# Kernel tuning notes

Hardware: AMD Instinct MI355X
Metric: run time of the kernel (lower is better)

The kernel has to match this reference:

```python
import jax, jax.numpy as jnp
import numpy as np

N, E, HS, HBS, L, SH, RBF, T, NZ, NH = 1024, 16384, 128, 32, 5, 25, 32, 50, 10, 4
HD = HS // NH
OUT = 14  # 3x0e + 2x1e + 1x2e -> 3 + 6 + 5
_rng = np.random.default_rng(7)
# fixed Clebsch-Gordan-style coupling tensor and expansion coefficients (deterministic constants)
CG = jnp.asarray((0.1 * _rng.normal(size=(SH, SH, SH))).astype(np.float32))
EXP = jnp.asarray((0.1 * _rng.normal(size=(SH, OUT, OUT))).astype(np.float32))
_SL = [(l * l, 2 * l + 1) for l in range(5)]  # per-l (offset, size) blocks in the 25-dim rep


def _real_sh(d):
    # real spherical harmonics l=0..4 of unit vectors d [E,3] -> [E,25]
    x, y, z = d[:, 0], d[:, 1], d[:, 2]
    x2, y2, z2 = x * x, y * y, z * z
    sh = [0.282095 * jnp.ones_like(x),
          0.488603 * y, 0.488603 * z, 0.488603 * x,
          1.092548 * x * y, 1.092548 * y * z, 0.315392 * (3 * z2 - 1), 1.092548 * x * z, 0.546274 * (x2 - y2),
          0.590044 * y * (3 * x2 - y2), 2.890611 * x * y * z, 0.457046 * y * (5 * z2 - 1),
          0.373176 * z * (5 * z2 - 3), 0.457046 * x * (5 * z2 - 1), 1.445306 * z * (x2 - y2),
          0.590044 * x * (x2 - 3 * y2),
          2.503343 * x * y * (x2 - y2), 1.770131 * y * z * (3 * x2 - y2), 0.946175 * x * y * (7 * z2 - 1),
          0.669047 * y * z * (7 * z2 - 3), 0.105786 * (35 * z2 * z2 - 30 * z2 + 3),
          0.669047 * x * z * (7 * z2 - 3), 0.473087 * (x2 - y2) * (7 * z2 - 1),
          1.770131 * x * z * (x2 - 3 * y2), 0.625836 * (x2 * x2 - 6 * x2 * y2 + y2 * y2)]
    return jnp.stack(sh, axis=-1)


def _rbf(r, cutoff=12.0, alpha=0.5):
    # exponential Bernstein radial basis with cosine cutoff, [E] -> [E,RBF]
    logf = np.concatenate([[0.0], np.cumsum(np.log(np.arange(1, RBF)))])
    logbinom = jnp.asarray((logf[RBF - 1] - logf - logf[::-1]).astype(np.float32))
    k = jnp.arange(RBF, dtype=jnp.float32)
    xr = jnp.exp(-alpha * r)[:, None]
    log1mx = jnp.log1p(-xr + 1e-7)
    b = jnp.exp(logbinom[None] + k[None] * (-alpha * r[:, None]) + (RBF - 1 - k)[None] * log1mx)
    fcut = 0.5 * (jnp.cos(jnp.pi * jnp.clip(r / cutoff, 0.0, 1.0)) + 1.0)
    return b * fcut[:, None]


def _mix(feat, W):
    # per-degree channel mixing: feat [*,C,25], W [5,C,D] -> [*,D,25]
    return jnp.concatenate([jnp.einsum('ncm,cd->ndm', feat[..., o:o + s], W[l])
                            for l, (o, s) in enumerate(_SL)], axis=-1)


def _forward(z, pos, edge_index, batch, t, step, embed, temb_T, temb_H, sig_W1, sig_b1, sig_W2, sig_b2,
             rad_W1, rad_b1, rad_W2, rad_b2, rad_W3, rad_b3, mix_W, Wq, Wk, Wii, Wij, path_ii, path_ij):
    n = z.shape[0]
    e = edge_index.shape[1]
    src, dst = edge_index[0], edge_index[1]
    vec = pos[src] - pos[dst]
    r = jnp.sqrt((vec * vec).sum(-1) + 1e-12)
    dvec = vec / r[:, None]
    rbf = _rbf(r)           # [E,32]
    sh = _real_sh(dvec)     # [E,25]
    nsc = embed[z]          # [N,HS]
    cat = jnp.concatenate([nsc, jnp.tile(temb_T[t][None], (n, 1)), jnp.tile(temb_H[step][None], (n, 1))], axis=-1)
    nsc = jax.nn.relu(cat @ sig_W1 + sig_b1) @ sig_W2 + sig_b2  # sigma_embedding
    x = jnp.zeros((n, HS, SH), jnp.float32).at[:, :, 0].set(nsc)  # scalar-initialized irrep features
    for l in range(L):
        # radial MLP -> per-edge per-channel tensor-product path weights
        h = jax.nn.silu(rbf @ rad_W1[l] + rad_b1[l])
        h = jax.nn.silu(h @ rad_W2[l] + rad_b2[l])
        w = h @ rad_W3[l] + rad_b3[l]                    # [E,HS]
        Tk = jnp.einsum('ej,ijk->eik', sh, CG)           # [E,25,25] CG-coupled SH operator
        msg = jnp.einsum('eci,eik->eck', x[src], Tk) * w[:, :, None]  # per-edge TP message [E,HS,25]
        agg = jax.ops.segment_sum(msg, dst, num_segments=n)
        y = _mix(agg, mix_W[l])
        # equivariant edge attention (scalars drive logits, full irreps are values)
        q = (x[:, :, 0] @ Wq[l]).reshape(n, NH, HD)
        kk = (x[:, :, 0] @ Wk[l]).reshape(n, NH, HD)
        logits = (q[dst] * kk[src]).sum(-1) * (1.0 / float(np.sqrt(HD)))  # [E,NH]
        m = jax.ops.segment_max(logits, dst, num_segments=n)
        m = jnp.where(jnp.isfinite(m), m, 0.0)
        a = jnp.exp(logits - m[dst])
        den = jax.ops.segment_sum(a, dst, num_segments=n)
        alpha = a / (den[dst] + 1e-9)
        v = x[src].reshape(e, NH, HD, SH)
        att = jax.ops.segment_sum(alpha[:, :, None, None] * v, dst, num_segments=n).reshape(n, HS, SH)
        x = x + y + att
        # gate nonlinearity: ssp/silu on scalars, sigmoid gate on higher-l blocks
        g = jax.nn.sigmoid(x[:, :, 0:1])
        x = jnp.concatenate([jax.nn.silu(x[:, :, 0:1]), x[:, :, 1:] * g], axis=-1)
    # expansion to hamiltonian blocks (3x0e+2x1e+1x2e -> 14x14)
    fii = _mix(x, Wii)                    # [N,HBS,25]
    fij = _mix(x[src] + x[dst], Wij)      # [E,HBS,25]
    w_ii = nsc @ path_ii                  # [N,HBS] path weights
    w_ij = jnp.concatenate([nsc[src], nsc[dst]], axis=-1) @ path_ij  # [E,HBS]
    H_ii = jnp.einsum('nd,ndm,mpq->npq', w_ii, fii, EXP)  # [N,14,14]
    H_ij = jnp.einsum('ed,edm,mpq->epq', w_ij, fij, EXP)  # [E,14,14]
    return H_ii, H_ij


def setup_inputs() -> dict:
    key = jax.random.key(0)
    ks = jax.random.split(key, 40)
    def nrm(i, shape, s):
        return (jax.random.normal(ks[i], shape) * s).astype(jnp.float32)
    inp = {}
    inp['z'] = jax.random.randint(ks[0], (N,), 0, NZ)
    inp['pos'] = nrm(1, (N, 3), 3.0)
    inp['edge_index'] = jax.random.randint(ks[2], (2, E), 0, N)
    inp['batch'] = jnp.sort(jax.random.randint(ks[3], (N,), 0, 8))
    inp['t'] = 25
    inp['step'] = 10
    inp['embed'] = nrm(4, (NZ, HS), 1.0)
    inp['temb_T'] = nrm(5, (T, HS), 1.0)
    inp['temb_H'] = nrm(6, (T, HS), 1.0)
    inp['sig_W1'] = nrm(7, (3 * HS, HS), (3 * HS) ** -0.5)
    inp['sig_b1'] = jnp.zeros((HS,), jnp.float32)
    inp['sig_W2'] = nrm(8, (HS, HS), HS ** -0.5)
    inp['sig_b2'] = jnp.zeros((HS,), jnp.float32)
    inp['rad_W1'] = nrm(9, (L, RBF, 64), RBF ** -0.5)
    inp['rad_b1'] = jnp.zeros((L, 64), jnp.float32)
    inp['rad_W2'] = nrm(10, (L, 64, 64), 64 ** -0.5)
    inp['rad_b2'] = jnp.zeros((L, 64), jnp.float32)
    inp['rad_W3'] = nrm(11, (L, 64, HS), 64 ** -0.5)
    inp['rad_b3'] = jnp.zeros((L, HS), jnp.float32)
    inp['mix_W'] = nrm(12, (L, 5, HS, HS), HS ** -0.5)
    inp['Wq'] = nrm(13, (L, HS, HS), HS ** -0.5)
    inp['Wk'] = nrm(14, (L, HS, HS), HS ** -0.5)
    inp['Wii'] = nrm(15, (5, HS, HBS), HS ** -0.5)
    inp['Wij'] = nrm(16, (5, HS, HBS), HS ** -0.5)
    inp['path_ii'] = nrm(17, (HS, HBS), HS ** -0.5)
    inp['path_ij'] = nrm(18, (2 * HS, HBS), (2 * HS) ** -0.5)
    return inp


def reference(z, pos, edge_index, batch, t, step, embed, temb_T, temb_H, sig_W1, sig_b1, sig_W2, sig_b2,
              rad_W1, rad_b1, rad_W2, rad_b2, rad_W3, rad_b3, mix_W, Wq, Wk, Wii, Wij, path_ii, path_ij):
    return _forward(z, pos, edge_index, batch, t, step, embed, temb_T, temb_H, sig_W1, sig_b1, sig_W2, sig_b2,
                    rad_W1, rad_b1, rad_W2, rad_b2, rad_W3, rad_b3, mix_W, Wq, Wk, Wii, Wij, path_ii, path_ij)
```

## Files before the change

kernel.cpp:

```cpp
#include <hip/hip_runtime.h>
#include <cstdint>
#include <cmath>
#include <cstddef>

constexpr int NN   = 1024;
constexpr int NE   = 16384;
constexpr int HSZ  = 128;
constexpr int NSH  = 25;
constexpr int NRBF = 32;
constexpr int NLAY = 5;
constexpr int XSZ  = HSZ * NSH;
constexpr int HII_SZ = NN * 196;
constexpr int TKP  = 800;


constexpr size_t OFF_CONSTS = 0;
constexpr size_t OFF_X    = 20560;
constexpr size_t OFF_AGG  = OFF_X    + (size_t)NN * XSZ;
constexpr size_t OFF_ATT  = OFF_AGG  + (size_t)NN * XSZ;
constexpr size_t OFF_X0   = OFF_ATT  + (size_t)NN * XSZ;
constexpr size_t OFF_NSC  = OFF_X0   + (size_t)NN * HSZ;
constexpr size_t OFF_Q    = OFF_NSC  + (size_t)NN * HSZ;
constexpr size_t OFF_K    = OFF_Q    + (size_t)NN * HSZ;
constexpr size_t OFF_RBF  = OFF_K    + (size_t)NN * HSZ;
constexpr size_t OFF_SH   = OFF_RBF  + (size_t)NE * NRBF;
constexpr size_t OFF_TK   = OFF_SH   + (size_t)NE * NSH;
constexpr size_t OFF_WRAD = OFF_TK   + (size_t)NE * TKP;
constexpr size_t OFF_INT  = OFF_WRAD + (size_t)NE * HSZ;
constexpr size_t NEED_BYTES = OFF_INT * 4 + (size_t)(1024 + 1025 + 1024 + 16384) * 4;

namespace qhc {

struct Pcg64 {
  unsigned __int128 state, inc;
  static unsigned __int128 mult() {
    return (((unsigned __int128)2549297995355413924ULL) << 64) | 4865540595714422341ULL;
  }
  void step() { state = state * mult() + inc; }
  uint64_t next64() {
    step();
    uint64_t hi = (uint64_t)(state >> 64), lo = (uint64_t)state;
    uint64_t x = hi ^ lo;
    unsigned rot = (unsigned)(state >> 122);
    return (x >> rot) | (x << ((64u - rot) & 63u));
  }
  double nextd() { return (double)(next64() >> 11) * (1.0 / 9007199254740992.0); }
};

struct HostConsts {
  float buf[20560];
  HostConsts() {
    const uint32_t INIT_A = 0x43b0d7e5u, MULT_A = 0x931e8875u;
    const uint32_t INIT_B = 0x8b51f9ddu, MULT_B = 0x58f38dedu;
    uint32_t pool[4];
    uint32_t hc = INIT_A;
    auto hashf = [&](uint32_t v) -> uint32_t {
      v ^= hc; hc *= MULT_A; v *= hc; v ^= v >> 16; return v;
    };
    auto mixf = [](uint32_t x, uint32_t y) -> uint32_t {
      uint32_t r = x * 0xca01f9ddu - y * 0x4973f715u;
      r ^= r >> 16;
      return r;
    };
    pool[0] = hashf(7u);
    for (int i = 1; i < 4; i++) pool[i] = hashf(0u);
    for (int s = 0; s < 4; s++)
      for (int d = 0; d < 4; d++)
        if (s != d) pool[d] = mixf(pool[d], hashf(pool[s]));
    uint32_t st32[8];
    uint32_t hb = INIT_B;
    for (int i = 0; i < 8; i++) {
      uint32_t v = pool[i % 4];
      v ^= hb; hb *= MULT_B; v *= hb; v ^= v >> 16;
      st32[i] = v;
    }
    uint64_t w0 = st32[0] | ((uint64_t)st32[1] << 32);
    uint64_t w1 = st32[2] | ((uint64_t)st32[3] << 32);
    uint64_t w2 = st32[4] | ((uint64_t)st32[5] << 32);
    uint64_t w3 = st32[6] | ((uint64_t)st32[7] << 32);
    unsigned __int128 seed = (((unsigned __int128)w0) << 64) | w1;
    unsigned __int128 incs = (((unsigned __int128)w2) << 64) | w3;
    Pcg64 g;
    g.state = 0; g.inc = (incs << 1) | 1;
    g.step(); g.state += seed; g.step();
    double wi[256], fi[256]; uint64_t ki[256];
    {
      const double m1 = 4503599627370496.0;
      double dn = 3.6541528853610087963519472518, tn = dn, vn = 0.00492867323399941;
      double q = vn / std::exp(-0.5 * dn * dn);
      ki[0] = (uint64_t)((dn / q) * m1); ki[1] = 0;
      wi[0] = q / m1; wi[255] = dn / m1;
      fi[0] = 1.0; fi[255] = std::exp(-0.5 * dn * dn);
      for (int i = 254; i >= 1; i--) {
        dn = std::sqrt(-2.0 * std::log(vn / dn + std::exp(-0.5 * dn * dn)));
        ki[i + 1] = (uint64_t)((dn / tn) * m1);
        tn = dn;
        fi[i] = std::exp(-0.5 * dn * dn);
        wi[i] = dn / m1;
      }
    }
    const double ZR = 3.6541528853610087963519472518;
    const double ZIR = 0.27366123732975827203338247596;
    auto stdnorm = [&]() -> double {
      for (;;) {
        uint64_t r = g.next64();
        int idx = (int)(r & 0xff);
        r >>= 8;
        int sign = (int)(r & 1);
        uint64_t rabs = (r >> 1) & 0x000fffffffffffffULL;
        double xv = (double)rabs * wi[idx];
        if (sign) xv = -xv;
        if (rabs < ki[idx]) return xv;
        if (idx == 0) {
          for (;;) {
            double xx = -ZIR * std::log1p(-g.nextd());
            double yy = -std::log1p(-g.nextd());
            if (yy + yy > xx * xx)
              return ((rabs >> 8) & 1) ? -(ZR + xx) : (ZR + xx);
          }
        } else {
          if (((fi[idx - 1] - fi[idx]) * g.nextd() + fi[idx]) < std::exp(-0.5 * xv * xv))
            return xv;
        }
      }
    };
    for (int i = 0; i < 15625 + 4900; i++) buf[i] = (float)(0.1 * stdnorm());
    double logf[32]; logf[0] = 0.0;
    for (int i = 1; i < 32; i++) logf[i] = logf[i - 1] + std::log((double)i);
    for (int k = 0; k < 32; k++) buf[15625 + 4900 + k] = (float)(logf[31] - logf[k] - logf[31 - k]);
    buf[20557] = buf[20558] = buf[20559] = 0.f;
  }
};
static HostConsts g_hc;
}

__device__ __forceinline__ float siluf(float a) { return a / (1.f + expf(-a)); }

__global__ __launch_bounds__(256) void qh_geom(
    const float* __restrict__ pos, const int* __restrict__ ei,
    const float* __restrict__ lbn, float* __restrict__ rbf, float* __restrict__ sh) {
  int e = blockIdx.x * 256 + threadIdx.x;
  if (e >= NE) return;
  int s = ei[e], d = ei[NE + e];
  float vx = pos[s * 3 + 0] - pos[d * 3 + 0];
  float vy = pos[s * 3 + 1] - pos[d * 3 + 1];
  float vz = pos[s * 3 + 2] - pos[d * 3 + 2];
  float r = sqrtf(vx * vx + vy * vy + vz * vz + 1e-12f);
  float inv = 1.0f / r;
  float x = vx * inv, y = vy * inv, z = vz * inv;
  float x2 = x * x, y2 = y * y, z2 = z * z;
  float* sp = sh + (size_t)e * NSH;
  sp[0] = 0.282095f;
  sp[1] = 0.488603f * y;
  sp[2] = 0.488603f * z;
  sp[3] = 0.488603f * x;
  sp[4] = 1.092548f * x * y;
  sp[5] = 1.092548f * y * z;
  sp[6] = 0.315392f * (3.f * z2 - 1.f);
  sp[7] = 1.092548f * x * z;
  sp[8] = 0.546274f * (x2 - y2);
  sp[9] = 0.590044f * y * (3.f * x2 - y2);
  sp[10] = 2.890611f * x * y * z;
  sp[11] = 0.457046f * y * (5.f * z2 - 1.f);
  sp[12] = 0.373176f * z * (5.f * z2 - 3.f);
  sp[13] = 0.457046f * x * (5.f * z2 - 1.f);
  sp[14] = 1.445306f * z * (x2 - y2);
  sp[15] = 0.590044f * x * (x2 - 3.f * y2);
  sp[16] = 2.503343f * x * y * (x2 - y2);
  sp[17] = 1.770131f * y * z * (3.f * x2 - y2);
  sp[18] = 0.946175f * x * y * (7.f * z2 - 1.f);
  sp[19] = 0.669047f * y * z * (7.f * z2 - 3.f);
  sp[20] = 0.105786f * (35.f * z2 * z2 - 30.f * z2 + 3.f);
  sp[21] = 0.669047f * x * z * (7.f * z2 - 3.f);
  sp[22] = 0.473087f * (x2 - y2) * (7.f * z2 - 1.f);
  sp[23] = 1.770131f * x * z * (x2 - 3.f * y2);
  sp[24] = 0.625836f * (x2 * x2 - 6.f * x2 * y2 + y2 * y2);
  float xr = expf(-0.5f * r);
  float l1 = log1pf(-xr + 1e-7f);
  float fc = 0.5f * (cosf(3.14159265358979323846f * fminf(r * (1.0f / 12.0f), 1.0f)) + 1.0f);
  float* rp = rbf + (size_t)e * NRBF;
  for (int k = 0; k < NRBF; k++) {
    float b = expf(lbn[k] + (float)k * (-0.5f * r) + (float)(NRBF - 1 - k) * l1);
    rp[k] = b * fc;
  }
}

__global__ __launch_bounds__(256) void qh_tk(
    const float* __restrict__ sh, const float* __restrict__ CG, float* __restrict__ Tkp) {
  __shared__ float shl[32 * NSH];
  int e0 = blockIdx.x * 32;
  int t = threadIdx.x;
  for (int i = t; i < 32 * NSH; i += 256) shl[i] = sh[(size_t)e0 * NSH + i];
  for (int i = t; i < 32 * TKP; i += 256) Tkp[(size_t)e0 * TKP + i] = 0.f;
  __syncthreads();
  for (int ik = t; ik < NSH * NSH; ik += 256) {
    int i = ik / NSH, k = ik % NSH;
    int pos = i * 32 + k + (k >= 7) + 2 * (k >= 13) + 2 * (k >= 19);
    float cg[NSH];
#pragma unroll
    for (int j = 0; j < NSH; j++) cg[j] = CG[i * 625 + j * NSH + k];
    for (int ee = 0; ee < 32; ee++) {
      float acc = 0.f;
#pragma unroll
      for (int j = 0; j < NSH; j++) acc += shl[ee * NSH + j] * cg[j];
      Tkp[(size_t)(e0 + ee) * TKP + pos] = acc;
    }
  }
}

__global__ __launch_bounds__(128) void qh_nsc(
    const int* __restrict__ z, const int* __restrict__ tptr, const int* __restrict__ sptr,
    const float* __restrict__ embed, const float* __restrict__ tT, const float* __restrict__ tH,
    const float* __restrict__ W1, const float* __restrict__ b1,
    const float* __restrict__ W2, const float* __restrict__ b2,
    float* __restrict__ nsc, float* __restrict__ x, float* __restrict__ x0) {
  __shared__ float cat[384];
  __shared__ float h[128];
  int nd = blockIdx.x, d = threadIdx.x;
  int zz = z[nd], tt = tptr[0], st = sptr[0];
  cat[d] = embed[zz * HSZ + d];
  cat[128 + d] = tT[tt * HSZ + d];
  cat[256 + d] = tH[st * HSZ + d];
  __syncthreads();
  float a = b1[d];
  for (int c = 0; c < 384; c++) a += cat[c] * W1[c * HSZ + d];
  h[d] = fmaxf(a, 0.f);
  __syncthreads();
  a = b2[d];
  for (int c = 0; c < 128; c++) a += h[c] * W2[c * HSZ + d];
  nsc[nd * HSZ + d] = a;
  x0[nd * HSZ + d] = a;
  float* xr = x + (size_t)nd * XSZ + d;
  xr[0] = a;
  for (int m = 1; m < NSH; m++) xr[m * 128] = 0.f;
}

__global__ __launch_bounds__(256) void qh_zero(int* counts) {
  int i = blockIdx.x * 256 + threadIdx.x;
  if (i < NN) counts[i] = 0;
}
__global__ __launch_bounds__(256) void qh_count(const int* __restrict__ ei, int* counts) {
  int e = blockIdx.x * 256 + threadIdx.x;
  if (e < NE) atomicAdd(&counts[ei[NE + e]], 1);
}
__global__ __launch_bounds__(1024) void qh_scan(const int* __restrict__ counts,
                                                int* starts, int* cursor) {
  __shared__ int tmp[NN];
  int t = threadIdx.x;
  tmp[t] = counts[t];
  __syncthreads();
  for (int ofs = 1; ofs < NN; ofs <<= 1) {
    int v = (t >= ofs) ? tmp[t - ofs] : 0;
    __syncthreads();
    tmp[t] += v;
    __syncthreads();
  }
  starts[t + 1] = tmp[t];
  if (t == 0) starts[0] = 0;
  cursor[t] = (t == 0) ? 0 : tmp[t - 1];
}
__global__ __launch_bounds__(256) void qh_scatter(const int* __restrict__ ei,
                                                  int* cursor, int* perm) {
  int e = blockIdx.x * 256 + threadIdx.x;
  if (e < NE) {
    int d = ei[NE + e];
    int pos = atomicAdd(&cursor[d], 1);
    perm[pos] = e;
  }
}

__global__ __launch_bounds__(256) void qh_rad(
    const float* __restrict__ rbf,
    const float* __restrict__ W1, const float* __restrict__ b1,
    const float* __restrict__ W2, const float* __restrict__ b2,
    const float* __restrict__ W3, const float* __restrict__ b3,
    float* __restrict__ wrad) {
  __shared__ float w1l[2048], w2l[4096], w3l[8192];
  __shared__ float rl[4][32], h1[4][64], h2[4][64];
  int t = threadIdx.x;
  for (int i = t; i < 2048; i += 256) w1l[i] = W1[i];
  for (int i = t; i < 4096; i += 256) w2l[i] = W2[i];
  for (int i = t; i < 8192; i += 256) w3l[i] = W3[i];
  __syncthreads();
  int e0 = blockIdx.x * 16;
  for (int q = 0; q < 4; q++) {
    int eb = e0 + q * 4;
    if (t < 128) rl[t >> 5][t & 31] = rbf[(size_t)(eb + (t >> 5)) * NRBF + (t & 31)];
    __syncthreads();
    {
      int eg = t >> 6, u = t & 63;
      float a = b1[u];
      for (int c = 0; c < 32; c++) a += rl[eg][c] * w1l[c * 64 + u];
      h1[eg][u] = siluf(a);
    }
    __syncthreads();
    {
      int eg = t >> 6, u = t & 63;
      float a = b2[u];
      for (int c = 0; c < 64; c++) a += h1[eg][c] * w2l[c * 64 + u];
      h2[eg][u] = siluf(a);
    }
    __syncthreads();
#pragma unroll
    for (int p = 0; p < 2; p++) {
      int eg = (t >> 7) + p * 2, u = t & 127;
      float a = b3[u];
      for (int c = 0; c < 64; c++) a += h2[eg][c] * w3l[c * 128 + u];
      wrad[(size_t)(eb + eg) * HSZ + u] = a;
    }
    __syncthreads();
  }
}

__global__ __launch_bounds__(256) void qh_qk(
    const float* __restrict__ x0, const float* __restrict__ Wq, const float* __restrict__ Wk,
    float* __restrict__ q, float* __restrict__ kk) {
  __shared__ float xl[128];
  int nd = blockIdx.x, t = threadIdx.x;
  if (t < 128) xl[t] = x0[nd * HSZ + t];
  __syncthreads();
  int d = t & 127;
  const float* W = (t < 128) ? Wq : Wk;
  float a = 0.f;
  for (int c = 0; c < 128; c++) a += xl[c] * W[c * HSZ + d];
  if (t < 128) q[nd * HSZ + d] = a;
  else kk[nd * HSZ + d] = a;
}

__global__ __launch_bounds__(256) void qh_logit(
    const float* __restrict__ q, const float* __restrict__ kk,
    const int* __restrict__ ei, float* __restrict__ logits) {
  int t = threadIdx.x;
  int e = blockIdx.x * 2 + (t >> 7);
  int c = t & 127;
  int s = ei[e], d = ei[NE + e];
  float p = q[d * HSZ + c] * kk[s * HSZ + c];
#pragma unroll
  for (int m = 16; m >= 1; m >>= 1) p += __shfl_xor(p, m);
  if ((c & 31) == 0) logits[e * 4 + (c >> 5)] = p * 0.17677669529663687f;
}

__global__ __launch_bounds__(64) void qh_soft(
    const float* __restrict__ logits, const int* __restrict__ starts,
    const int* __restrict__ perm, float* __restrict__ alpha) {
  int nd = blockIdx.x, t = threadIdx.x;
  int hh = t >> 4, l = t & 15;
  int jb = starts[nd], je = starts[nd + 1];
  float m = -1e30f;
  for (int j = jb + l; j < je; j += 16) m = fmaxf(m, logits[perm[j] * 4 + hh]);
#pragma unroll
  for (int s = 1; s < 16; s <<= 1) m = fmaxf(m, __shfl_xor(m, s));
  float den = 0.f;
  for (int j = jb + l; j < je; j += 16) den += expf(logits[perm[j] * 4 + hh] - m);
#pragma unroll
  for (int s = 1; s < 16; s <<= 1) den += __shfl_xor(den, s);
  float inv = 1.f / (den + 1e-9f);
  for (int j = jb + l; j < je; j += 16) {
    int e = perm[j];
    alpha[e * 4 + hh] = expf(logits[e * 4 + hh] - m) * inv;
  }
}

__global__ __launch_bounds__(256, 8) void qh_msgatt(
    const float* __restrict__ x, const float* __restrict__ Tkp,
    const float* __restrict__ wrad, const float* __restrict__ alpha,
    const int* __restrict__ starts, const int* __restrict__ perm,
    const int* __restrict__ ei,
    float* __restrict__ agg, float* __restrict__ att) {
  __shared__ float xs[2][1600];
  __shared__ float wl[2][64];
  int nd = blockIdx.x >> 1, h = blockIdx.x & 1;
  int t = threadIdx.x;
  int cl = t & 63, q4 = t >> 6;
  int q4u = __builtin_amdgcn_readfirstlane(q4);
  int c = h * 64 + cl;
  int k0 = (q4 == 0) ? 0 : (1 + 6 * q4);
  int nk = (q4 == 0) ? 7 : 6;
  float am[7], aa[7];
#pragma unroll
  for (int u = 0; u < 7; u++) { am[u] = 0.f; aa[u] = 0.f; }
  int jb = starts[nd], je = starts[nd + 1];

  float rx[7], rw = 0.f;
  if (jb < je) {
    int e = perm[jb], s = ei[e];
#pragma unroll
    for (int u = 0; u < 6; u++) {
      int i = t + u * 256;
      rx[u] = x[(size_t)s * XSZ + (i >> 6) * 128 + h * 64 + (i & 63)];
    }
    if (t < 64) rx[6] = x[(size_t)s * XSZ + 24 * 128 + h * 64 + t];
    if (t < 64) rw = wrad[(size_t)e * HSZ + h * 64 + t];
#pragma unroll
    for (int u = 0; u < 6; u++) xs[0][t + u * 256] = rx[u];
    if (t < 64) xs[0][1536 + t] = rx[6];
    if (t < 64) wl[0][t] = rw;
  }
  __syncthreads();
  for (int j = jb; j < je; j++) {
    int cur = (j - jb) & 1, nxt = cur ^ 1;
    int e = perm[j];
    int eu = __builtin_amdgcn_readfirstlane(e);
    const float* tkr = Tkp + (size_t)eu * TKP + q4u * 8;
    float al = alpha[e * 4 + (c >> 5)];
    bool more = (j + 1 < je);
    if (more) {
      int e2 = perm[j + 1], s2 = ei[e2];
#pragma unroll
      for (int u = 0; u < 6; u++) {
        int i = t + u * 256;
        rx[u] = x[(size_t)s2 * XSZ + (i >> 6) * 128 + h * 64 + (i & 63)];
      }
      if (t < 64) rx[6] = x[(size_t)s2 * XSZ + 24 * 128 + h * 64 + t];
      if (t < 64) rw = wrad[(size_t)e2 * HSZ + h * 64 + t];
    }
    float wc = wl[cur][cl];
#pragma unroll 5
    for (int i = 0; i < NSH; i++) {
      float xw = xs[cur][i * 64 + cl] * wc;
      float4 t0 = *(const float4*)(tkr + i * 32);
      float4 t1 = *(const float4*)(tkr + i * 32 + 4);
      am[0] += xw * t0.x; am[1] += xw * t0.y; am[2] += xw * t0.z; am[3] += xw * t0.w;
      am[4] += xw * t1.x; am[5] += xw * t1.y; am[6] += xw * t1.z;
    }
#pragma unroll
    for (int u = 0; u < 7; u++)
      if (u < nk) aa[u] += al * xs[cur][(k0 + u) * 64 + cl];
    __syncthreads();
    if (more) {
#pragma unroll
      for (int u = 0; u < 6; u++) xs[nxt][t + u * 256] = rx[u];
      if (t < 64) xs[nxt][1536 + t] = rx[6];
      if (t < 64) wl[nxt][t] = rw;
    }
    __syncthreads();
  }
#pragma unroll
  for (int u = 0; u < 7; u++)
    if (u < nk) {
      agg[(size_t)nd * XSZ + (k0 + u) * 128 + c] = am[u];
      att[(size_t)nd * XSZ + (k0 + u) * 128 + c] = aa[u];
    }
}

__global__ __launch_bounds__(256) void qh_mixgemm(
    const float* __restrict__ mixW, float* __restrict__ agg) {
  __shared__ float Wl[8192];
  __shared__ float Al[4096];
  int b = blockIdx.x, t = threadIdx.x;
  int lb, cum;
  if (b < 32)       { lb = 0; cum = 0; }
  else if (b < 128) { lb = 1; cum = 32; }
  else if (b < 288) { lb = 2; cum = 128; }
  else if (b < 512) { lb = 3; cum = 288; }
  else              { lb = 4; cum = 512; }
  int sl = 2 * lb + 1, o = lb * lb;
  int row0 = (b - cum) * 32;
  const float* W = mixW + lb * 16384;
  for (int i = t; i < 4096; i += 256) {
    int r = i >> 7, cc = i & 127;
    int gr = row0 + r, n = gr / sl, m = o + gr - n * sl;
    Al[i] = agg[(size_t)n * XSZ + m * 128 + cc];
  }
  int dl = t & 63, rg = t >> 6;
  float out[2][8];
  for (int p = 0; p < 2; p++) {
    __syncthreads();
    for (int i = t; i < 8192; i += 256) {
      int cc = i >> 6, d2 = i & 63;
      Wl[i] = W[cc * 128 + p * 64 + d2];
    }
    __syncthreads();
    float acc[8];
#pragma unroll
    for (int r = 0; r < 8; r++) acc[r] = 0.f;
    for (int cc = 0; cc < 128; cc++) {
      float w = Wl[cc * 64 + dl];
#pragma unroll
      for (int r = 0; r < 8; r++) acc[r] += Al[(rg * 8 + r) * 128 + cc] * w;
    }
#pragma unroll
    for (int r = 0; r < 8; r++) out[p][r] = acc[r];
  }
#pragma unroll
  for (int p = 0; p < 2; p++)
#pragma unroll
    for (int r = 0; r < 8; r++) {
      int gr = row0 + rg * 8 + r, n = gr / sl, m = o + gr - n * sl;
      agg[(size_t)n * XSZ + m * 128 + p * 64 + dl] = out[p][r];
    }
}

__global__ __launch_bounds__(256) void qh_gate(
    const float* __restrict__ y, const float* __restrict__ att,
    float* __restrict__ x, float* __restrict__ x0) {
  __shared__ float v0l[128];
  int nd = blockIdx.x, t = threadIdx.x;
  int d = t & 127, mh = t >> 7;
  int m0 = mh ? 13 : 0, nm = mh ? 12 : 13;
  float v[13];
  size_t base = (size_t)nd * XSZ + (size_t)m0 * 128 + d;
#pragma unroll
  for (int u = 0; u < 13; u++)
    if (u < nm) v[u] = x[base + (size_t)u * 128] + y[base + (size_t)u * 128] + att[base + (size_t)u * 128];
  if (mh == 0) v0l[d] = v[0];
  __syncthreads();
  float g = 1.f / (1.f + expf(-v0l[d]));
#pragma unroll
  for (int u = 0; u < 13; u++)
    if (u < nm) x[base + (size_t)u * 128] = v[u] * g;
  if (mh == 0) x0[nd * HSZ + d] = v[0] * g;
}

__global__ __launch_bounds__(256) void qh_prep(
    const float* __restrict__ x, const float* __restrict__ nsc,
    const float* __restrict__ Wii, const float* __restrict__ Wij,
    const float* __restrict__ pii, const float* __restrict__ pij,
    const float* __restrict__ EXPc,
    float* __restrict__ fm, float* __restrict__ awb, float* __restrict__ out) {
  __shared__ float xl[XSZ];
  __shared__ float nl[128];
  __shared__ float wc[4096];
  __shared__ float fml[800];
  __shared__ float wiil[32];
  __shared__ float gl[25];
  int nd = blockIdx.x, t = threadIdx.x;
  for (int i = t; i < XSZ; i += 256) xl[i] = x[(size_t)nd * XSZ + i];
  if (t < 128) nl[t] = nsc[nd * HSZ + t];
  __syncthreads();
  if (t < 32) {
    float a = 0.f;
    for (int cc = 0; cc < 128; cc++) a += nl[cc] * pii[cc * 32 + t];
    wiil[t] = a;
  } else if (t < 96) {
    int d = (t - 32) & 31;
    int half = (t - 32) >> 5;
    const float* pp = pij + (half ? 128 * 32 : 0);
    float a = 0.f;
    for (int cc = 0; cc < 128; cc++) a += nl[cc] * pp[cc * 32 + d];
    awb[nd * 64 + half * 32 + d] = a;
  }
  for (int lb = 0; lb < 5; lb++) {
    __syncthreads();
    for (int i = t; i < 4096; i += 256) wc[i] = Wii[lb * 4096 + i];
    __syncthreads();
    int o = lb * lb, sl = 2 * lb + 1;
    for (int idx = t; idx < 32 * sl; idx += 256) {
      int d = idx & 31, m = o + (idx >> 5);
      float a = 0.f;
      for (int cc = 0; cc < 128; cc++) a += xl[m * 128 + cc] * wc[cc * 32 + d];
      fml[d * NSH + m] = a;
    }
  }
  __syncthreads();
  if (t < 25) {
    float a = 0.f;
#pragma unroll
    for (int d = 0; d < 32; d++) a += wiil[d] * fml[d * NSH + t];
    gl[t] = a;
  }
  __syncthreads();
  if (t < 196) {
    float a = 0.f;
#pragma unroll
    for (int m = 0; m < 25; m++) a += gl[m] * EXPc[m * 196 + t];
    out[(size_t)nd * 196 + t] = a;
  }
  for (int lb = 0; lb < 5; lb++) {
    __syncthreads();
    for (int i = t; i < 4096; i += 256) wc[i] = Wij[lb * 4096 + i];
    __syncthreads();
    int o = lb * lb, sl = 2 * lb + 1;
    for (int idx = t; idx < 32 * sl; idx += 256) {
      int d = idx & 31, m = o + (idx >> 5);
      float a = 0.f;
      for (int cc = 0; cc < 128; cc++) a += xl[m * 128 + cc] * wc[cc * 32 + d];
      fm[(size_t)nd * 800 + d * NSH + m] = a;
    }
  }
}

__global__ __launch_bounds__(256) void qh_fij2(
    const int* __restrict__ ei, const float* __restrict__ fm,
    const float* __restrict__ awb, const float* __restrict__ EXPc,
    float* __restrict__ out) {
  __shared__ float fsum[800], wsum[32], gl[25];
  int e = blockIdx.x, t = threadIdx.x;
  int s = ei[e], d2 = ei[NE + e];
  for (int i = t; i < 800; i += 256)
    fsum[i] = fm[(size_t)s * 800 + i] + fm[(size_t)d2 * 800 + i];
  if (t < 32) wsum[t] = awb[s * 64 + t] + awb[d2 * 64 + 32 + t];
  __syncthreads();
  if (t < 25) {
    float a = 0.f;
#pragma unroll
    for (int d = 0; d < 32; d++) a += wsum[d] * fsum[d * NSH + t];
    gl[t] = a;
  }
  __syncthreads();
  if (t < 196) {
    float a = 0.f;
#pragma unroll
    for (int m = 0; m < 25; m++) a += gl[m] * EXPc[m * 196 + t];
    out[HII_SZ + (size_t)e * 196 + t] = a;
  }
}

extern "C" void kernel_launch(void* const* d_in, const int* in_sizes, int n_in,
                              void* d_out, int out_size, void* d_ws, size_t ws_size,
                              hipStream_t stream) {
  (void)in_sizes; (void)n_in; (void)out_size;
  if (ws_size < NEED_BYTES) return;

  const int*   z    = (const int*)d_in[0];
  const float* pos  = (const float*)d_in[1];
  const int*   ei   = (const int*)d_in[2];
  const int*   tptr = (const int*)d_in[4];
  const int*   sptr = (const int*)d_in[5];
  const float* embed= (const float*)d_in[6];
  const float* tT   = (const float*)d_in[7];
  const float* tH   = (const float*)d_in[8];
  const float* sW1  = (const float*)d_in[9];
  const float* sb1  = (const float*)d_in[10];
  const float* sW2  = (const float*)d_in[11];
  const float* sb2  = (const float*)d_in[12];
  const float* rW1  = (const float*)d_in[13];
  const float* rb1  = (const float*)d_in[14];
  const float* rW2  = (const float*)d_in[15];
  const float* rb2  = (const float*)d_in[16];
  const float* rW3  = (const float*)d_in[17];
  const float* rb3  = (const float*)d_in[18];
  const float* mixW = (const float*)d_in[19];
  const float* Wq   = (const float*)d_in[20];
  const float* Wk   = (const float*)d_in[21];
  const float* Wii  = (const float*)d_in[22];
  const float* Wij  = (const float*)d_in[23];
  const float* pii  = (const float*)d_in[24];
  const float* pij  = (const float*)d_in[25];

  float* ws = (float*)d_ws;
  float* CGd   = ws + OFF_CONSTS;
  float* EXPd  = CGd + 15625;
  float* LBNd  = CGd + 15625 + 4900;
  float* x     = ws + OFF_X;
  float* agg   = ws + OFF_AGG;
  float* att   = ws + OFF_ATT;
  float* x0    = ws + OFF_X0;
  float* nsc   = ws + OFF_NSC;
  float* qarr  = ws + OFF_Q;
  float* karr  = ws + OFF_K;
  float* rbf   = ws + OFF_RBF;
  float* sh    = ws + OFF_SH;
  float* Tkp   = ws + OFF_TK;
  float* wrad  = ws + OFF_WRAD;
  float* logits = ws + OFF_SH;
  float* alphaA = ws + OFF_SH + 65536;
  float* fm     = ws + OFF_AGG;
  float* awb    = ws + OFF_AGG + 819200;
  int* ibase   = (int*)(ws + OFF_INT);
  int* counts  = ibase;
  int* starts  = ibase + 1024;
  int* cursor  = ibase + 1024 + 1025;
  int* perm    = ibase + 1024 + 1025 + 1024;
  float* outp  = (float*)d_out;

  hipMemcpyAsync(CGd, qhc::g_hc.buf, 20557 * sizeof(float), hipMemcpyHostToDevice, stream);

  qh_geom<<<NE / 256, 256, 0, stream>>>(pos, ei, LBNd, rbf, sh);
  qh_tk<<<NE / 32, 256, 0, stream>>>(sh, CGd, Tkp);
  qh_nsc<<<NN, 128, 0, stream>>>(z, tptr, sptr, embed, tT, tH, sW1, sb1, sW2, sb2, nsc, x, x0);
  qh_zero<<<NN / 256, 256, 0, stream>>>(counts);
  qh_count<<<NE / 256, 256, 0, stream>>>(ei, counts);
  qh_scan<<<1, 1024, 0, stream>>>(counts, starts, cursor);
  qh_scatter<<<NE / 256, 256, 0, stream>>>(ei, cursor, perm);

  for (int l = 0; l < NLAY; l++) {
    qh_rad<<<NE / 16, 256, 0, stream>>>(rbf,
        rW1 + (size_t)l * 32 * 64, rb1 + (size_t)l * 64,
        rW2 + (size_t)l * 64 * 64, rb2 + (size_t)l * 64,
        rW3 + (size_t)l * 64 * 128, rb3 + (size_t)l * 128, wrad);
    qh_qk<<<NN, 256, 0, stream>>>(x0, Wq + (size_t)l * 16384, Wk + (size_t)l * 16384, qarr, karr);
    qh_logit<<<NE / 2, 256, 0, stream>>>(qarr, karr, ei, logits);
    qh_soft<<<NN, 64, 0, stream>>>(logits, starts, perm, alphaA);
    qh_msgatt<<<NN * 2, 256, 0, stream>>>(x, Tkp, wrad, alphaA, starts, perm, ei, agg, att);
    qh_mixgemm<<<800, 256, 0, stream>>>(mixW + (size_t)l * 81920, agg);
    qh_gate<<<NN, 256, 0, stream>>>(agg, att, x, x0);
  }

  qh_prep<<<NN, 256, 0, stream>>>(x, nsc, Wii, Wij, pii, pij, EXPd, fm, awb, outp);
  qh_fij2<<<NE, 256, 0, stream>>>(ei, fm, awb, EXPd, outp);
}
```

Measured before the change: 1.353 ms.

## Read source features directly from global memory in message-attention kernel

```diff
diff --git a/kernel.cpp b/kernel.cpp
--- a/kernel.cpp
+++ b/kernel.cpp
@@ -367,8 +367,6 @@
     const int* __restrict__ starts, const int* __restrict__ perm,
     const int* __restrict__ ei,
     float* __restrict__ agg, float* __restrict__ att) {
-  __shared__ float xs[2][1600];
-  __shared__ float wl[2][64];
   int nd = blockIdx.x >> 1, h = blockIdx.x & 1;
   int t = threadIdx.x;
   int cl = t & 63, q4 = t >> 6;
@@ -380,44 +378,19 @@
 #pragma unroll
   for (int u = 0; u < 7; u++) { am[u] = 0.f; aa[u] = 0.f; }
   int jb = starts[nd], je = starts[nd + 1];
-
-  float rx[7], rw = 0.f;
-  if (jb < je) {
-    int e = perm[jb], s = ei[e];
-#pragma unroll
-    for (int u = 0; u < 6; u++) {
-      int i = t + u * 256;
-      rx[u] = x[(size_t)s * XSZ + (i >> 6) * 128 + h * 64 + (i & 63)];
-    }
-    if (t < 64) rx[6] = x[(size_t)s * XSZ + 24 * 128 + h * 64 + t];
-    if (t < 64) rw = wrad[(size_t)e * HSZ + h * 64 + t];
-#pragma unroll
-    for (int u = 0; u < 6; u++) xs[0][t + u * 256] = rx[u];
-    if (t < 64) xs[0][1536 + t] = rx[6];
-    if (t < 64) wl[0][t] = rw;
-  }
-  __syncthreads();
+  const float* xb = x + c;
+
   for (int j = jb; j < je; j++) {
-    int cur = (j - jb) & 1, nxt = cur ^ 1;
     int e = perm[j];
     int eu = __builtin_amdgcn_readfirstlane(e);
+    int s = ei[e];
     const float* tkr = Tkp + (size_t)eu * TKP + q4u * 8;
+    const float* xr = xb + (size_t)s * XSZ;
     float al = alpha[e * 4 + (c >> 5)];
-    bool more = (j + 1 < je);
-    if (more) {
-      int e2 = perm[j + 1], s2 = ei[e2];
-#pragma unroll
-      for (int u = 0; u < 6; u++) {
-        int i = t + u * 256;
-        rx[u] = x[(size_t)s2 * XSZ + (i >> 6) * 128 + h * 64 + (i & 63)];
-      }
-      if (t < 64) rx[6] = x[(size_t)s2 * XSZ + 24 * 128 + h * 64 + t];
-      if (t < 64) rw = wrad[(size_t)e2 * HSZ + h * 64 + t];
-    }
-    float wc = wl[cur][cl];
+    float wc = wrad[(size_t)e * HSZ + c];
 #pragma unroll 5
     for (int i = 0; i < NSH; i++) {
-      float xw = xs[cur][i * 64 + cl] * wc;
+      float xw = xr[i * 128] * wc;
       float4 t0 = *(const float4*)(tkr + i * 32);
       float4 t1 = *(const float4*)(tkr + i * 32 + 4);
       am[0] += xw * t0.x; am[1] += xw * t0.y; am[2] += xw * t0.z; am[3] += xw * t0.w;
@@ -425,15 +398,7 @@
     }
 #pragma unroll
     for (int u = 0; u < 7; u++)
-      if (u < nk) aa[u] += al * xs[cur][(k0 + u) * 64 + cl];
-    __syncthreads();
-    if (more) {
-#pragma unroll
-      for (int u = 0; u < 6; u++) xs[nxt][t + u * 256] = rx[u];
-      if (t < 64) xs[nxt][1536 + t] = rx[6];
-      if (t < 64) wl[nxt][t] = rw;
-    }
-    __syncthreads();
+      if (u < nk) aa[u] += al * xr[(k0 + u) * 128];
   }
 #pragma unroll
   for (int u = 0; u < 7; u++)
```

Result: no change. 1.364 ms (+0.8%).
